# Optimization experiments

Measured on AMD Instinct MI355X. Metric: run time of the kernel, lower is better.

Reference implementation:

```python
import jax, jax.numpy as jnp
import numpy as np

B, S, D, H = 4, 2048, 512, 8
KD = D // H          # key_dim == head_dim == 64
FFN = 4 * D

def _ln(x, g, b, eps):
    mu = x.mean(-1, keepdims=True)
    var = ((x - mu) ** 2).mean(-1, keepdims=True)
    return (x - mu) / jnp.sqrt(var + eps) * g + b

def setup_inputs():
    key = jax.random.key(0)
    ks = jax.random.split(key, 8)
    def lin(k, o, i, scale=0.02):
        k1, k2 = jax.random.split(k)
        return (jax.random.normal(k1, (o, i), jnp.float32) * scale,
                jax.random.normal(k2, (o,), jnp.float32) * scale)
    wq, bq = lin(ks[0], D, D)
    wk, bk = lin(ks[1], D, D)
    wv, bv = lin(ks[2], D, D)
    wg, bg = lin(ks[3], D, D)
    wo, bo = lin(ks[4], D, D)
    fc1_w, fc1_b = lin(ks[5], FFN, D)
    fc2_w, fc2_b = lin(ks[6], D, FFN)
    return {
        'src': jax.random.normal(ks[7], (B, S, D), jnp.float32),
        'mask': jnp.zeros((S, S), jnp.bool_),
        'padding_mask': jnp.zeros((B, S), jnp.bool_),
        'wq': wq, 'bq': bq, 'wk': wk, 'bk': bk, 'wv': wv, 'bv': bv,
        'wg': wg, 'bg': bg, 'wo': wo, 'bo': bo,
        'fc1_w': fc1_w, 'fc1_b': fc1_b, 'fc2_w': fc2_w, 'fc2_b': fc2_b,
        'ln_ffn_g': jnp.ones((FFN,), jnp.float32), 'ln_ffn_b': jnp.zeros((FFN,), jnp.float32),
        'n0_g': jnp.ones((D,), jnp.float32), 'n0_b': jnp.zeros((D,), jnp.float32),
        'n1_g': jnp.ones((D,), jnp.float32), 'n1_b': jnp.zeros((D,), jnp.float32),
    }

def reference(src, mask, padding_mask, wq, bq, wk, bk, wv, bv, wg, bg, wo, bo,
              fc1_w, fc1_b, fc2_w, fc2_b, ln_ffn_g, ln_ffn_b, n0_g, n0_b, n1_g, n1_b):
    b, s, d = src.shape
    # RetNet per-head decay mask (h, s, s): exp((i-j)*log(gamma_h)) on the lower triangle,
    # row-normalized by sqrt(row sum) (torchscale RetNetRelPos, parallel mode).
    idx = jnp.arange(s)
    diff = (idx[:, None] - idx[None, :]).astype(src.dtype)
    decay = jnp.log(1.0 - 2.0 ** (-5.0 - jnp.arange(H, dtype=src.dtype)))
    dm = jnp.where(diff[None] >= 0, jnp.exp(diff[None] * decay[:, None, None]), 0.0)
    dm = dm / jnp.sqrt(dm.sum(-1, keepdims=True))
    # projections; k scaled by key_dim**-0.5 before head split
    q = (src @ wq.T + bq).reshape(b, s, H, KD).transpose(0, 2, 1, 3)
    k = ((src @ wk.T + bk) * (KD ** -0.5)).reshape(b, s, H, KD).transpose(0, 2, 1, 3)
    v = src @ wv.T + bv
    g = src @ wg.T + bg
    # parallel retention: additive decay bias, detached L1 row normalization
    qk = jnp.einsum('bhid,bhjd->bhij', q, k) + dm[None]
    den = jnp.maximum(jnp.abs(jax.lax.stop_gradient(qk).sum(-1, keepdims=True)), 1.0)
    qk = qk / den
    vr = v.reshape(b, s, H, KD).transpose(0, 2, 1, 3)
    o = jnp.einsum('bhij,bhjd->bhid', qk, vr).transpose(0, 2, 1, 3)  # (b,s,h,hd)
    # per-head LayerNorm, eps=1e-6, no affine
    mu = o.mean(-1, keepdims=True)
    o = (o - mu) / jnp.sqrt(((o - mu) ** 2).mean(-1, keepdims=True) + 1e-6)
    o = jax.nn.silu(g) * o.reshape(b, s, d)
    o = o @ wo.T + bo
    # post-norm residual layout
    x = _ln(src + o, n0_g, n0_b, 1e-5)
    h = jax.nn.gelu(x @ fc1_w.T + fc1_b, approximate=False)
    h = _ln(h, ln_ffn_g, ln_ffn_b, 1e-6)  # subln
    h = h @ fc2_w.T + fc2_b
    return _ln(x + h, n1_g, n1_b, 1e-5)
```

## Files before the change

kernel.cpp:

```cpp
#include <hip/hip_runtime.h>
#include <hip/hip_bf16.h>
#include <math.h>

#define DEV __device__ __forceinline__

typedef __attribute__((ext_vector_type(4))) float f32x4;
typedef __attribute__((ext_vector_type(16))) float f32x16;
typedef __attribute__((ext_vector_type(8))) short bf16x8;
typedef __attribute__((ext_vector_type(8))) unsigned short u16x8;
typedef unsigned short u16;
typedef unsigned int u32;

DEV u16 f2bf(float f) {
  union { float f; u32 u; } v; v.f = f;
  u32 r = v.u + 0x7fffu + ((v.u >> 16) & 1u);
  return (u16)(r >> 16);
}
DEV float bf2f(u16 h) {
  union { u32 u; float f; } v; v.u = ((u32)h) << 16;
  return v.f;
}
DEV float bfel(bf16x8 v, int e) {
  union { bf16x8 b; u16x8 u; } x; x.b = v; return bf2f(x.u[e]);
}

DEV void gl_lds16(const u16* g, u16* s) {
  __builtin_amdgcn_global_load_lds((const __attribute__((address_space(1))) void*)g,
                                   (__attribute__((address_space(3))) void*)s, 16, 0, 0);
}

DEV void barrier_() {
  __builtin_amdgcn_sched_barrier(0);
  asm volatile("" ::: "memory");
  __builtin_amdgcn_s_barrier();
  asm volatile("" ::: "memory");
  __builtin_amdgcn_sched_barrier(0);
}

#define MFMA16(a, b, c) __builtin_amdgcn_mfma_f32_16x16x32_bf16((a), (b), (c), 0, 0, 0)
#define MFMA32(a, b, c) __builtin_amdgcn_mfma_f32_32x32x16_bf16((a), (b), (c), 0, 0, 0)

DEV void cast8(const float* in, u16* out, float s) {
  f32x4 a = *(const f32x4*)in;
  f32x4 b = *(const f32x4*)(in + 4);
  u16x8 r;
  r[0] = f2bf(a[0] * s); r[1] = f2bf(a[1] * s); r[2] = f2bf(a[2] * s); r[3] = f2bf(a[3] * s);
  r[4] = f2bf(b[0] * s); r[5] = f2bf(b[1] * s); r[6] = f2bf(b[2] * s); r[7] = f2bf(b[3] * s);
  *(u16x8*)out = r;
}

__global__ __launch_bounds__(256) void prep_cast(
    const float* __restrict__ src, const float* __restrict__ wq, const float* __restrict__ wk,
    const float* __restrict__ wv, const float* __restrict__ wg, const float* __restrict__ wo,
    const float* __restrict__ fc1, const float* __restrict__ fc2,
    const float* __restrict__ bq, const float* __restrict__ bk,
    const float* __restrict__ bv, const float* __restrict__ bg,
    u16* __restrict__ src_bf, u16* __restrict__ Wcat, u16* __restrict__ wo_bf,
    u16* __restrict__ fc1_bf, u16* __restrict__ fc2_bf, float* __restrict__ bcat) {
  int u = blockIdx.x * 256 + threadIdx.x;
  if (u < 524288) {
    cast8(src + (size_t)u * 8, src_bf + (size_t)u * 8, 1.0f);
  } else if (u < 557056) {
    int v = u - 524288; cast8(wq + (size_t)v * 8, Wcat + (size_t)v * 8, 1.0f);
  } else if (u < 589824) {
    int v = u - 557056; cast8(wk + (size_t)v * 8, Wcat + 262144 + (size_t)v * 8, 0.125f);
  } else if (u < 622592) {
    int v = u - 589824; cast8(wv + (size_t)v * 8, Wcat + 524288 + (size_t)v * 8, 1.0f);
  } else if (u < 655360) {
    int v = u - 622592; cast8(wg + (size_t)v * 8, Wcat + 786432 + (size_t)v * 8, 1.0f);
  } else if (u < 688128) {
    int v = u - 655360; cast8(wo + (size_t)v * 8, wo_bf + (size_t)v * 8, 1.0f);
  } else if (u < 819200) {
    int v = u - 688128; cast8(fc1 + (size_t)v * 8, fc1_bf + (size_t)v * 8, 1.0f);
  } else if (u < 950272) {
    int v = u - 819200; cast8(fc2 + (size_t)v * 8, fc2_bf + (size_t)v * 8, 1.0f);
  } else if (u < 950528) {
    int v = u - 950272;
    #pragma unroll
    for (int e = 0; e < 8; e++) {
      int c = v * 8 + e;
      float val;
      if (c < 512)       val = bq[c];
      else if (c < 1024) val = bk[c - 512] * 0.125f;
      else if (c < 1536) val = bv[c - 1024];
      else               val = bg[c - 1536];
      bcat[c] = val;
    }
  }
}

template <int ACT>
__global__ __launch_bounds__(256) void gemm_v3(
    const u16* __restrict__ A, const u16* __restrict__ W, const float* __restrict__ bias,
    u16* __restrict__ Ob, int N, int K, int TN) {
  __shared__ __align__(16) u16 sm[2][16384];
  const int t = threadIdx.x, l = t & 63;
  const int w = t >> 6, wr = (w >> 1) * 64, wc = (w & 1) * 64;
  const int lc = l & 15, lch = l >> 4;
  const int NT = K >> 6;

  const int orig = blockIdx.x;
  const int cpx = gridDim.x >> 3;
  const int sid = (orig & 7) * cpx + (orig >> 3);
  const int bm = (sid / TN) * 128, bn = (sid % TN) * 128;

  const int srow = t >> 3, sc8 = t & 7;
  const u16* stA = A + (size_t)(bm + srow) * K + ((sc8 ^ (srow & 7)) * 8);
  const u16* stB = W + (size_t)(bn + srow) * K + ((sc8 ^ (srow & 7)) * 8);

#define STAGE(bidx, kt)                                                        \
  {                                                                            \
    u16* d = (u16*)sm[bidx] + t * 8;                                           \
    _Pragma("unroll")                                                          \
    for (int j = 0; j < 4; j++)                                                \
      gl_lds16(stA + (size_t)j * 32 * K + (kt), d + j * 2048);                 \
    _Pragma("unroll")                                                          \
    for (int j = 0; j < 4; j++)                                                \
      gl_lds16(stB + (size_t)j * 32 * K + (kt), d + 8192 + j * 2048);          \
  }

  f32x4 acc[4][4] = {};

  STAGE(0, 0)

  for (int tt = 0; tt < NT; ++tt) {
    if (tt + 1 < NT) {
      STAGE((tt + 1) & 1, (tt + 1) * 64)
      asm volatile("s_waitcnt vmcnt(8)" ::: "memory");
    } else {
      asm volatile("s_waitcnt vmcnt(0)" ::: "memory");
    }
    barrier_();
    const u16* bufp = sm[tt & 1];
    bf16x8 af[4][2], bfv[4][2];
    #pragma unroll
    for (int mi = 0; mi < 4; mi++) {
      const int row = wr + mi * 16 + lc;
      #pragma unroll
      for (int ks = 0; ks < 2; ks++) {
        const int ch = ks * 4 + lch;
        af[mi][ks] = *(const bf16x8*)&bufp[row * 64 + ((ch ^ (row & 7)) * 8)];
      }
    }
    #pragma unroll
    for (int ni = 0; ni < 4; ni++) {
      const int row = wc + ni * 16 + lc;
      #pragma unroll
      for (int ks = 0; ks < 2; ks++) {
        const int ch = ks * 4 + lch;
        bfv[ni][ks] = *(const bf16x8*)&bufp[8192 + row * 64 + ((ch ^ (row & 7)) * 8)];
      }
    }
    #pragma unroll
    for (int ks = 0; ks < 2; ks++)
      #pragma unroll
      for (int mi = 0; mi < 4; mi++)
        #pragma unroll
        for (int ni = 0; ni < 4; ni++)
          acc[mi][ni] = MFMA16(af[mi][ks], bfv[ni][ks], acc[mi][ni]);
    asm volatile("s_waitcnt lgkmcnt(0)" ::: "memory");
    barrier_();
  }
#undef STAGE

  u16* osm = (u16*)sm;
  #pragma unroll
  for (int ni = 0; ni < 4; ni++) {
    const int col = wc + ni * 16 + lc;
    const float bb = bias[bn + col];
    const int ckey = col >> 3, clow = col & 7;
    #pragma unroll
    for (int mi = 0; mi < 4; mi++) {
      #pragma unroll
      for (int r = 0; r < 4; r++) {
        const int row = wr + mi * 16 + lch * 4 + r;
        float v = acc[mi][ni][r] + bb;
        if (ACT == 1) v = 0.5f * v * (1.0f + erff(v * 0.70710678118f));
        osm[row * 128 + ((ckey ^ ((row & 7) << 1)) << 3) + clow] = f2bf(v);
      }
    }
  }
  __syncthreads();
  #pragma unroll
  for (int p = 0; p < 8; p++) {
    const int flat = p * 256 + t;
    const int row = flat >> 4, c = flat & 15;
    u16x8 y = *(const u16x8*)&osm[row * 128 + ((c ^ ((row & 7) << 1)) << 3)];
    *(u16x8*)&Ob[(size_t)(bm + row) * N + bn + c * 8] = y;
  }
}

template <int ACT>
__global__ __launch_bounds__(256) void gemm_m64(
    const u16* __restrict__ A, const u16* __restrict__ W, const float* __restrict__ bias,
    u16* __restrict__ Ob, int N, int K, int TN) {
  __shared__ __align__(16) u16 sm[2][12288];
  const int t = threadIdx.x, l = t & 63;
  const int w = t >> 6, wr = (w >> 1) * 32, wc = (w & 1) * 64;
  const int lc = l & 15, lch = l >> 4;
  const int NT = K >> 6;

  const int orig = blockIdx.x;
  const int cpx = gridDim.x >> 3;
  const int sid = (orig & 7) * cpx + (orig >> 3);
  const int bm = (sid / TN) * 64, bn = (sid % TN) * 128;

  const int srow = t >> 3, sc8 = t & 7;
  const u16* stA = A + (size_t)(bm + srow) * K + ((sc8 ^ (srow & 7)) * 8);
  const u16* stB = W + (size_t)(bn + srow) * K + ((sc8 ^ (srow & 7)) * 8);

#define STAGE(bidx, kt)                                                        \
  {                                                                            \
    u16* d = (u16*)sm[bidx] + t * 8;                                           \
    _Pragma("unroll")                                                          \
    for (int j = 0; j < 2; j++)                                                \
      gl_lds16(stA + (size_t)j * 32 * K + (kt), d + j * 2048);                 \
    _Pragma("unroll")                                                          \
    for (int j = 0; j < 4; j++)                                                \
      gl_lds16(stB + (size_t)j * 32 * K + (kt), d + 4096 + j * 2048);          \
  }

  f32x4 acc[2][4] = {};

  STAGE(0, 0)

  for (int tt = 0; tt < NT; ++tt) {
    if (tt + 1 < NT) {
      STAGE((tt + 1) & 1, (tt + 1) * 64)
      asm volatile("s_waitcnt vmcnt(6)" ::: "memory");
    } else {
      asm volatile("s_waitcnt vmcnt(0)" ::: "memory");
    }
    barrier_();
    const u16* bufp = sm[tt & 1];
    bf16x8 af[2][2], bfv[4][2];
    #pragma unroll
    for (int mi = 0; mi < 2; mi++) {
      const int row = wr + mi * 16 + lc;
      #pragma unroll
      for (int ks = 0; ks < 2; ks++) {
        const int ch = ks * 4 + lch;
        af[mi][ks] = *(const bf16x8*)&bufp[row * 64 + ((ch ^ (row & 7)) * 8)];
      }
    }
    #pragma unroll
    for (int ni = 0; ni < 4; ni++) {
      const int row = wc + ni * 16 + lc;
      #pragma unroll
      for (int ks = 0; ks < 2; ks++) {
        const int ch = ks * 4 + lch;
        bfv[ni][ks] = *(const bf16x8*)&bufp[4096 + row * 64 + ((ch ^ (row & 7)) * 8)];
      }
    }
    #pragma unroll
    for (int ks = 0; ks < 2; ks++)
      #pragma unroll
      for (int mi = 0; mi < 2; mi++)
        #pragma unroll
        for (int ni = 0; ni < 4; ni++)
          acc[mi][ni] = MFMA16(af[mi][ks], bfv[ni][ks], acc[mi][ni]);
    asm volatile("s_waitcnt lgkmcnt(0)" ::: "memory");
    barrier_();
  }
#undef STAGE

  u16* osm = (u16*)sm;
  #pragma unroll
  for (int ni = 0; ni < 4; ni++) {
    const int col = wc + ni * 16 + lc;
    const float bb = bias[bn + col];
    const int ckey = col >> 3, clow = col & 7;
    #pragma unroll
    for (int mi = 0; mi < 2; mi++) {
      #pragma unroll
      for (int r = 0; r < 4; r++) {
        const int row = wr + mi * 16 + lch * 4 + r;
        float v = acc[mi][ni][r] + bb;
        if (ACT == 1) v = 0.5f * v * (1.0f + erff(v * 0.70710678118f));
        osm[row * 128 + ((ckey ^ ((row & 7) << 1)) << 3) + clow] = f2bf(v);
      }
    }
  }
  __syncthreads();
  #pragma unroll
  for (int p = 0; p < 4; p++) {
    const int flat = p * 256 + t;
    const int row = flat >> 4, c = flat & 15;
    u16x8 y = *(const u16x8*)&osm[row * 128 + ((c ^ ((row & 7) << 1)) << 3)];
    *(u16x8*)&Ob[(size_t)(bm + row) * N + bn + c * 8] = y;
  }
}

__global__ __launch_bounds__(256) void transkv(
    const u16* __restrict__ qkvg, u16* __restrict__ ktg, u16* __restrict__ vtg,
    float* __restrict__ Wtab) {
  __shared__ u16 Lk[64 * 72], Lv[64 * 72];
  const int t = threadIdx.x;
  const int bh = blockIdx.x, c = blockIdx.y, b = bh >> 3, h = bh & 7;
  const int jt = c * 64;
  const u16* kptr = qkvg + (size_t)(b * 2048 + jt) * 2048 + 512 + h * 64;
  const u16* vptr = kptr + 512;
  const int r0 = t >> 3, c0 = (t & 7) * 8;
  u16x8 k0 = *(const u16x8*)(kptr + (size_t)r0 * 2048 + c0);
  u16x8 k1 = *(const u16x8*)(kptr + (size_t)(r0 + 32) * 2048 + c0);
  u16x8 v0 = *(const u16x8*)(vptr + (size_t)r0 * 2048 + c0);
  u16x8 v1 = *(const u16x8*)(vptr + (size_t)(r0 + 32) * 2048 + c0);
  #pragma unroll
  for (int e = 0; e < 8; e++) {
    Lk[(c0 + e) * 72 + r0] = k0[e];  Lk[(c0 + e) * 72 + 32 + r0] = k1[e];
    Lv[(c0 + e) * 72 + r0] = v0[e];  Lv[(c0 + e) * 72 + 32 + r0] = v1[e];
  }
  __syncthreads();
  {
    u16* kd = ktg + (size_t)bh * 64 * 2048 + jt;
    u16* vd = vtg + (size_t)bh * 64 * 2048 + jt;
    *(u16x8*)(kd + (size_t)r0 * 2048 + c0)        = *(const u16x8*)&Lk[r0 * 72 + c0];
    *(u16x8*)(kd + (size_t)(r0 + 32) * 2048 + c0) = *(const u16x8*)&Lk[(r0 + 32) * 72 + c0];
    *(u16x8*)(vd + (size_t)r0 * 2048 + c0)        = *(const u16x8*)&Lv[r0 * 72 + c0];
    *(u16x8*)(vd + (size_t)(r0 + 32) * 2048 + c0) = *(const u16x8*)&Lv[(r0 + 32) * 72 + c0];
  }
  if (t < 64) {
    const float gamma = 1.0f - exp2f(-5.0f - (float)h);
    float acc = 0.0f, p = 1.0f;
    for (int jj = 0; jj < 64; jj++) {
      acc += p * bf2f(Lv[t * 72 + (63 - jj)]);
      p *= gamma;
    }
    Wtab[((size_t)bh * 32 + c) * 64 + t] = acc;
  }
}

__global__ __launch_bounds__(256) void scanvtk(
    const u16* __restrict__ ktg, const u16* __restrict__ vtg,
    float* __restrict__ Ctab, float* __restrict__ ksum, u16* __restrict__ vtk) {
  __shared__ float red[3][4096];
  const int t = threadIdx.x, l = t & 63, w = t >> 6;
  const int bh = blockIdx.x, h = bh & 7;
  const int lc = l & 15, lch = l >> 4;

  {
    const int a = t & 63, q = t >> 6;
    const u16* kr = ktg + (size_t)bh * 64 * 2048 + (size_t)a * 2048 + q * 512;
    float s = 0.0f;
    for (int j = 0; j < 512; j += 8) {
      u16x8 v = *(const u16x8*)(kr + j);
      #pragma unroll
      for (int e = 0; e < 8; e++) s += bf2f(v[e]);
    }
    red[0][q * 64 + a] = s;
  }
  __syncthreads();
  if (t < 64) {
    ksum[bh * 64 + t] = red[0][t] + red[0][64 + t] + red[0][128 + t] + red[0][192 + t];
    const float gamma = 1.0f - exp2f(-5.0f - (float)h);
    const float g64 = exp2f(64.0f * log2f(gamma));
    float* Wp = Ctab + (size_t)bh * 32 * 64 + t;
    float C = 0.0f;
    for (int c = 0; c < 32; c++) {
      C = C * g64 + Wp[c * 64];
      Wp[c * 64] = C;
    }
  }

  const u16* vb = vtg + (size_t)bh * 64 * 2048;
  const u16* kb = ktg + (size_t)bh * 64 * 2048;
  f32x4 acc[4][4] = {};
  for (int it = 0; it < 16; ++it) {
    const int j0 = w * 512 + it * 32 + lch * 8;
    bf16x8 af[4], bfr[4];
    #pragma unroll
    for (int mt = 0; mt < 4; mt++)
      af[mt] = *(const bf16x8*)(vb + (size_t)(mt * 16 + lc) * 2048 + j0);
    #pragma unroll
    for (int nt = 0; nt < 4; nt++)
      bfr[nt] = *(const bf16x8*)(kb + (size_t)(nt * 16 + lc) * 2048 + j0);
    #pragma unroll
    for (int mt = 0; mt < 4; mt++)
      #pragma unroll
      for (int nt = 0; nt < 4; nt++)
        acc[mt][nt] = MFMA16(af[mt], bfr[nt], acc[mt][nt]);
  }
  __syncthreads();
  if (w > 0) {
    #pragma unroll
    for (int mt = 0; mt < 4; mt++)
      #pragma unroll
      for (int nt = 0; nt < 4; nt++)
        #pragma unroll
        for (int r = 0; r < 4; r++)
          red[w - 1][(mt * 16 + lch * 4 + r) * 64 + nt * 16 + lc] = acc[mt][nt][r];
  }
  __syncthreads();
  if (w == 0) {
    u16* out = vtk + (size_t)bh * 64 * 64;
    #pragma unroll
    for (int mt = 0; mt < 4; mt++)
      #pragma unroll
      for (int nt = 0; nt < 4; nt++)
        #pragma unroll
        for (int r = 0; r < 4; r++) {
          int row = mt * 16 + lch * 4 + r, col = nt * 16 + lc;
          float v = acc[mt][nt][r] + red[0][row * 64 + col] + red[1][row * 64 + col] +
                    red[2][row * 64 + col];
          out[row * 64 + col] = f2bf(v);
        }
  }
}

__global__ __launch_bounds__(512) void ret_out(
    const u16* __restrict__ qkvg, const u16* __restrict__ vtg,
    const u16* __restrict__ vtk, const float* __restrict__ Ctab,
    const float* __restrict__ ksum, u16* __restrict__ gated) {
  const int S = 2048, DD = 2048;
  const int bh = blockIdx.x, b = bh >> 3, h = bh & 7;
  const int t = threadIdx.x, l = t & 63, w = t >> 6;
  const int lid = l & 31, hi = l >> 5;
  const int wrow = blockIdx.y * 256 + w * 32;
  const int i_q = wrow + lid;
  const int chunk = wrow >> 6;
  const int iloc = i_q & 63;

  __shared__ __align__(16) u16 sm[18432];
  float* smf = (float*)sm;

  const size_t base = (size_t)b * S * DD + (size_t)h * 64;
  const u16* qp = qkvg + base;
  const u16* gp = qkvg + base + 1536;

  const float gamma = 1.0f - exp2f(-5.0f - (float)h);
  const float l2g = log2f(gamma);
  const float rowsum = (1.0f - exp2f((float)(i_q + 1) * l2g)) * exp2f(5.0f + (float)h);
  const float rrs = rsqrtf(rowsum);

  {
    const int il = t >> 3, j0 = (t & 7) * 8;
    u16x8 row;
    #pragma unroll
    for (int e = 0; e < 8; e++) {
      int d = il - (j0 + e);
      row[e] = (d >= 0) ? f2bf(exp2f((float)d * l2g)) : (u16)0;
    }
    *(u16x8*)&sm[il * 72 + j0] = row;
  }
  if (t < 256) {
    int cc = blockIdx.y * 4 - 1 + (t >> 6);
    smf[4608 + t] = (cc >= 0) ? Ctab[((size_t)bh * 32 + cc) * 64 + (t & 63)] : 0.0f;
  } else if (t < 320) {
    smf[4864 + (t - 256)] = ksum[bh * 64 + (t - 256)];
  }
  __syncthreads();

  bf16x8 qf[4];
  #pragma unroll
  for (int kc = 0; kc < 4; kc++)
    qf[kc] = *(const bf16x8*)(qp + (size_t)i_q * DD + kc * 16 + 8 * hi);

  const u16* vt_b = vtg + (size_t)bh * 64 * S;
  const u16* vk_b = vtk + (size_t)bh * 64 * 64;

  f32x16 accO0, accO1;
  #pragma unroll
  for (int r = 0; r < 16; r++) { accO0[r] = 0.0f; accO1[r] = 0.0f; }

  #pragma unroll
  for (int kc = 0; kc < 4; kc++) {
    bf16x8 lb = *(const bf16x8*)&sm[iloc * 72 + kc * 16 + hi * 8];
    bf16x8 va0 = *(const bf16x8*)(vt_b + (size_t)lid * S + chunk * 64 + kc * 16 + hi * 8);
    bf16x8 va1 = *(const bf16x8*)(vt_b + (size_t)(lid + 32) * S + chunk * 64 + kc * 16 + hi * 8);
    accO0 = MFMA32(va0, lb, accO0);
    accO1 = MFMA32(va1, lb, accO1);
  }
  {
    const float gpw = exp2f((float)(iloc + 1) * l2g);
    const float* Cst = &smf[4608 + (w >> 1) * 64];
    #pragma unroll
    for (int r = 0; r < 16; r++) {
      int br = (r & 3) + 8 * (r >> 2) + 4 * hi;
      accO0[r] += gpw * Cst[br];
      accO1[r] += gpw * Cst[32 + br];
    }
  }
  #pragma unroll
  for (int r = 0; r < 16; r++) { accO0[r] *= rrs; accO1[r] *= rrs; }
  #pragma unroll
  for (int kc = 0; kc < 4; kc++) {
    bf16x8 ka0 = *(const bf16x8*)(vk_b + (size_t)lid * 64 + kc * 16 + hi * 8);
    bf16x8 ka1 = *(const bf16x8*)(vk_b + (size_t)(lid + 32) * 64 + kc * 16 + hi * 8);
    accO0 = MFMA32(ka0, qf[kc], accO0);
    accO1 = MFMA32(ka1, qf[kc], accO1);
  }
  float dsum = 0.0f;
  #pragma unroll
  for (int kc = 0; kc < 4; kc++) {
    const float* Ks = &smf[4864 + kc * 16 + hi * 8];
    #pragma unroll
    for (int e = 0; e < 8; e++) dsum += bfel(qf[kc], e) * Ks[e];
  }
  dsum += __shfl_xor(dsum, 32);
  float den = dsum + sqrtf(rowsum);
  float rden = 1.0f / fmaxf(fabsf(den), 1.0f);

  float o0[16], o1[16];
  float s1 = 0.0f, s2 = 0.0f;
  #pragma unroll
  for (int r = 0; r < 16; r++) {
    o0[r] = accO0[r] * rden; s1 += o0[r]; s2 += o0[r] * o0[r];
    o1[r] = accO1[r] * rden; s1 += o1[r]; s2 += o1[r] * o1[r];
  }
  s1 += __shfl_xor(s1, 32);
  s2 += __shfl_xor(s2, 32);
  float mu = s1 * (1.0f / 64.0f);
  float var = s2 * (1.0f / 64.0f) - mu * mu;
  float rv = rsqrtf(var + 1e-6f);

  __syncthreads();

  u16* Ot = sm + w * 2304;
  #pragma unroll
  for (int r = 0; r < 16; r++) {
    int d = (r & 3) + 8 * (r >> 2) + 4 * hi;
    Ot[lid * 72 + d]      = f2bf((o0[r] - mu) * rv);
    Ot[lid * 72 + 32 + d] = f2bf((o1[r] - mu) * rv);
  }
  {
    const int i2 = l >> 1, half = l & 1;
    const int row = wrow + i2;
    #pragma unroll
    for (int c = 0; c < 4; c++) {
      u16x8 y8 = *(const u16x8*)&Ot[i2 * 72 + half * 32 + c * 8];
      u16x8 g8 = *(const u16x8*)(gp + (size_t)row * DD + half * 32 + c * 8);
      u16x8 o8;
      #pragma unroll
      for (int e = 0; e < 8; e++) {
        float gv = bf2f(g8[e]);
        float sg = gv / (1.0f + __expf(-gv));
        o8[e] = f2bf(bf2f(y8[e]) * sg);
      }
      *(u16x8*)&gated[((size_t)(b * S + row)) * 512 + h * 64 + half * 32 + c * 8] = o8;
    }
  }
}

template <int AF32, int WF>
__global__ __launch_bounds__(256) void add_lnT(
    const void* __restrict__ Ap, const u16* __restrict__ Bv,
    const float* __restrict__ gam, const float* __restrict__ bet, float eps,
    float* __restrict__ Of, u16* __restrict__ Ob) {
  int row = blockIdx.x * 4 + (threadIdx.x >> 6);
  int l = threadIdx.x & 63;
  float x[8];
  u16x8 cv = *(const u16x8*)(Bv + (size_t)row * 512 + l * 8);
  if (AF32) {
    const float* a = (const float*)Ap + (size_t)row * 512 + l * 8;
    f32x4 a0 = *(const f32x4*)a, a1 = *(const f32x4*)(a + 4);
    #pragma unroll
    for (int e = 0; e < 4; e++) { x[e] = a0[e] + bf2f(cv[e]); x[4 + e] = a1[e] + bf2f(cv[4 + e]); }
  } else {
    u16x8 av = *(const u16x8*)((const u16*)Ap + (size_t)row * 512 + l * 8);
    #pragma unroll
    for (int e = 0; e < 8; e++) x[e] = bf2f(av[e]) + bf2f(cv[e]);
  }
  float s = 0.f, s2 = 0.f;
  #pragma unroll
  for (int e = 0; e < 8; e++) { s += x[e]; s2 += x[e] * x[e]; }
  #pragma unroll
  for (int m = 1; m <= 32; m <<= 1) { s += __shfl_xor(s, m); s2 += __shfl_xor(s2, m); }
  float mu = s * (1.0f / 512.0f);
  float var = s2 * (1.0f / 512.0f) - mu * mu;
  float rinv = rsqrtf(var + eps);
  f32x4 g0 = *(const f32x4*)(gam + l * 8), g1 = *(const f32x4*)(gam + l * 8 + 4);
  f32x4 b0 = *(const f32x4*)(bet + l * 8), b1 = *(const f32x4*)(bet + l * 8 + 4);
  f32x4 y0, y1;
  #pragma unroll
  for (int e = 0; e < 4; e++) {
    y0[e] = (x[e] - mu) * rinv * g0[e] + b0[e];
    y1[e] = (x[4 + e] - mu) * rinv * g1[e] + b1[e];
  }
  if (WF) {
    float* op = Of + (size_t)row * 512 + l * 8;
    *(f32x4*)op = y0;
    *(f32x4*)(op + 4) = y1;
  }
  if (Ob) {
    u16x8 rb_;
    #pragma unroll
    for (int e = 0; e < 4; e++) { rb_[e] = f2bf(y0[e]); rb_[4 + e] = f2bf(y1[e]); }
    *(u16x8*)(Ob + (size_t)row * 512 + l * 8) = rb_;
  }
}

__global__ __launch_bounds__(256) void subln_ffn(
    u16* __restrict__ hbuf, const float* __restrict__ gam, const float* __restrict__ bet) {
  int row = blockIdx.x * 4 + (threadIdx.x >> 6);
  int l = threadIdx.x & 63;
  u16* p = hbuf + (size_t)row * 2048;
  float x[32];
  #pragma unroll
  for (int cch = 0; cch < 4; cch++) {
    u16x8 v = *(const u16x8*)(p + cch * 512 + l * 8);
    #pragma unroll
    for (int e = 0; e < 8; e++) x[cch * 8 + e] = bf2f(v[e]);
  }
  float s = 0.f, s2 = 0.f;
  #pragma unroll
  for (int e = 0; e < 32; e++) { s += x[e]; s2 += x[e] * x[e]; }
  #pragma unroll
  for (int m = 1; m <= 32; m <<= 1) { s += __shfl_xor(s, m); s2 += __shfl_xor(s2, m); }
  float mu = s * (1.0f / 2048.0f);
  float var = s2 * (1.0f / 2048.0f) - mu * mu;
  float rinv = rsqrtf(var + 1e-6f);
  #pragma unroll
  for (int cch = 0; cch < 4; cch++) {
    int col = cch * 512 + l * 8;
    f32x4 g0 = *(const f32x4*)(gam + col), g1 = *(const f32x4*)(gam + col + 4);
    f32x4 b0 = *(const f32x4*)(bet + col), b1 = *(const f32x4*)(bet + col + 4);
    u16x8 o;
    #pragma unroll
    for (int e = 0; e < 4; e++) {
      o[e]     = f2bf((x[cch * 8 + e]     - mu) * rinv * g0[e] + b0[e]);
      o[4 + e] = f2bf((x[cch * 8 + 4 + e] - mu) * rinv * g1[e] + b1[e]);
    }
    *(u16x8*)(p + col) = o;
  }
}

extern "C" void kernel_launch(void* const* d_in, const int* in_sizes, int n_in,
                              void* d_out, int out_size, void* d_ws, size_t ws_size,
                              hipStream_t stream) {
  const float* src  = (const float*)d_in[0];
  const float* wq   = (const float*)d_in[3];
  const float* bq   = (const float*)d_in[4];
  const float* wk   = (const float*)d_in[5];
  const float* bk   = (const float*)d_in[6];
  const float* wv   = (const float*)d_in[7];
  const float* bv   = (const float*)d_in[8];
  const float* wg   = (const float*)d_in[9];
  const float* bg   = (const float*)d_in[10];
  const float* wo   = (const float*)d_in[11];
  const float* bo   = (const float*)d_in[12];
  const float* fc1w = (const float*)d_in[13];
  const float* fc1b = (const float*)d_in[14];
  const float* fc2w = (const float*)d_in[15];
  const float* fc2b = (const float*)d_in[16];
  const float* lng  = (const float*)d_in[17];
  const float* lnb  = (const float*)d_in[18];
  const float* n0g  = (const float*)d_in[19];
  const float* n0b  = (const float*)d_in[20];
  const float* n1g  = (const float*)d_in[21];
  const float* n1b  = (const float*)d_in[22];

  if (ws_size < 91242496u) return;

  char* ws = (char*)d_ws;
  u16*   src_bf = (u16*)(ws + 0);
  u16*   Wcat   = (u16*)(ws + 8388608);
  u16*   wo_bf  = (u16*)(ws + 10485760);
  u16*   fc1_bf = (u16*)(ws + 11010048);
  u16*   fc2_bf = (u16*)(ws + 13107200);
  float* bcat   = (float*)(ws + 15204352);
  u16*   qkvg   = (u16*)(ws + 15212544);
  u16*   gated  = (u16*)(ws + 48766976);
  u16*   attn   = (u16*)(ws + 57155584);
  u16*   vtg    = (u16*)(ws + 65544192);
  u16*   ktg    = (u16*)(ws + 73932800);
  u16*   xbf    = (u16*)(ws + 82321408);
  float* Ctab   = (float*)(ws + 90710016);
  u16*   vtkb   = (u16*)(ws + 90972160);
  float* ksumb  = (float*)(ws + 91234304);

  prep_cast<<<3713, 256, 0, stream>>>(src, wq, wk, wv, wg, wo, fc1w, fc2w,
                                      bq, bk, bv, bg,
                                      src_bf, Wcat, wo_bf, fc1_bf, fc2_bf, bcat);
  gemm_v3<0><<<1024, 256, 0, stream>>>(src_bf, Wcat, bcat, qkvg, 2048, 512, 16);
  transkv<<<dim3(32, 32), 256, 0, stream>>>(qkvg, ktg, vtg, Ctab);
  scanvtk<<<32, 256, 0, stream>>>(ktg, vtg, Ctab, ksumb, vtkb);
  ret_out<<<dim3(32, 8), 512, 0, stream>>>(qkvg, vtg, vtkb, Ctab, ksumb, gated);
  gemm_m64<0><<<512, 256, 0, stream>>>(gated, wo_bf, bo, attn, 512, 512, 4);
  add_lnT<1, 0><<<2048, 256, 0, stream>>>(src, attn, n0g, n0b, 1e-5f, nullptr, xbf);
  gemm_v3<1><<<1024, 256, 0, stream>>>(xbf, fc1_bf, fc1b, qkvg, 2048, 512, 16);
  subln_ffn<<<2048, 256, 0, stream>>>(qkvg, lng, lnb);
  gemm_m64<0><<<512, 256, 0, stream>>>(qkvg, fc2_bf, fc2b, attn, 512, 2048, 4);
  add_lnT<0, 1><<<2048, 256, 0, stream>>>(xbf, attn, n1g, n1b, 1e-5f, (float*)d_out, nullptr);
}
```

Measured before the change: 178.9 us.

## Fuse K/V transpose into QKVG GEMM epilogue and move chunk decay sums into scan

The QKVG projection GEMM now writes its K and V column tiles directly in transposed (head, dim, seq) layout from shared memory, so the separate transkv kernel is removed. The per-chunk decayed V sums that transkv produced are now computed inside scanvtk from the transposed V. This saves a launch and one read/write pass over K and V. The cost is extra serial work in scanvtk, which runs only 32 blocks, and the K/V sections no longer get row-major output, which relies on nothing downstream reading K/V from qkvg.

```diff
diff --git a/kernel.cpp b/kernel.cpp
--- a/kernel.cpp
+++ b/kernel.cpp
@@ -89,10 +89,11 @@
   }
 }
 
-template <int ACT>
+template <int ACT, int TKV>
 __global__ __launch_bounds__(256) void gemm_v3(
     const u16* __restrict__ A, const u16* __restrict__ W, const float* __restrict__ bias,
-    u16* __restrict__ Ob, int N, int K, int TN) {
+    u16* __restrict__ Ob, u16* __restrict__ ktgp, u16* __restrict__ vtgp,
+    int N, int K, int TN) {
   __shared__ __align__(16) u16 sm[2][16384];
   const int t = threadIdx.x, l = t & 63;
   const int w = t >> 6, wr = (w >> 1) * 64, wc = (w & 1) * 64;
@@ -181,6 +182,30 @@
     }
   }
   __syncthreads();
+
+  if (TKV) {
+    const int sec = bn >> 9;
+    if (sec == 1 || sec == 2) {
+      u16* dst = (sec == 1) ? ktgp : vtgp;
+      const int bb2 = bm >> 11, s0 = bm & 2047;
+      const int hbase = (bn & 511) >> 6;
+      #pragma unroll
+      for (int pp = 0; pp < 8; pp++) {
+        const int pr = pp * 32 + (t >> 3);
+        const int col = pr >> 1, half = pr & 1, g = t & 7;
+        const int h = hbase + (col >> 6), d = col & 63;
+        const int ckey = col >> 3, clow = col & 7;
+        u16x8 v;
+        #pragma unroll
+        for (int e = 0; e < 8; e++) {
+          const int row = half * 64 + g * 8 + e;
+          v[e] = osm[row * 128 + ((ckey ^ (e << 1)) << 3) + clow];
+        }
+        *(u16x8*)(dst + ((size_t)((bb2 * 8 + h) * 64 + d)) * 2048 + s0 + half * 64 + g * 8) = v;
+      }
+      return;
+    }
+  }
   #pragma unroll
   for (int p = 0; p < 8; p++) {
     const int flat = p * 256 + t;
@@ -291,45 +316,6 @@
   }
 }
 
-__global__ __launch_bounds__(256) void transkv(
-    const u16* __restrict__ qkvg, u16* __restrict__ ktg, u16* __restrict__ vtg,
-    float* __restrict__ Wtab) {
-  __shared__ u16 Lk[64 * 72], Lv[64 * 72];
-  const int t = threadIdx.x;
-  const int bh = blockIdx.x, c = blockIdx.y, b = bh >> 3, h = bh & 7;
-  const int jt = c * 64;
-  const u16* kptr = qkvg + (size_t)(b * 2048 + jt) * 2048 + 512 + h * 64;
-  const u16* vptr = kptr + 512;
-  const int r0 = t >> 3, c0 = (t & 7) * 8;
-  u16x8 k0 = *(const u16x8*)(kptr + (size_t)r0 * 2048 + c0);
-  u16x8 k1 = *(const u16x8*)(kptr + (size_t)(r0 + 32) * 2048 + c0);
-  u16x8 v0 = *(const u16x8*)(vptr + (size_t)r0 * 2048 + c0);
-  u16x8 v1 = *(const u16x8*)(vptr + (size_t)(r0 + 32) * 2048 + c0);
-  #pragma unroll
-  for (int e = 0; e < 8; e++) {
-    Lk[(c0 + e) * 72 + r0] = k0[e];  Lk[(c0 + e) * 72 + 32 + r0] = k1[e];
-    Lv[(c0 + e) * 72 + r0] = v0[e];  Lv[(c0 + e) * 72 + 32 + r0] = v1[e];
-  }
-  __syncthreads();
-  {
-    u16* kd = ktg + (size_t)bh * 64 * 2048 + jt;
-    u16* vd = vtg + (size_t)bh * 64 * 2048 + jt;
-    *(u16x8*)(kd + (size_t)r0 * 2048 + c0)        = *(const u16x8*)&Lk[r0 * 72 + c0];
-    *(u16x8*)(kd + (size_t)(r0 + 32) * 2048 + c0) = *(const u16x8*)&Lk[(r0 + 32) * 72 + c0];
-    *(u16x8*)(vd + (size_t)r0 * 2048 + c0)        = *(const u16x8*)&Lv[r0 * 72 + c0];
-    *(u16x8*)(vd + (size_t)(r0 + 32) * 2048 + c0) = *(const u16x8*)&Lv[(r0 + 32) * 72 + c0];
-  }
-  if (t < 64) {
-    const float gamma = 1.0f - exp2f(-5.0f - (float)h);
-    float acc = 0.0f, p = 1.0f;
-    for (int jj = 0; jj < 64; jj++) {
-      acc += p * bf2f(Lv[t * 72 + (63 - jj)]);
-      p *= gamma;
-    }
-    Wtab[((size_t)bh * 32 + c) * 64 + t] = acc;
-  }
-}
-
 __global__ __launch_bounds__(256) void scanvtk(
     const u16* __restrict__ ktg, const u16* __restrict__ vtg,
     float* __restrict__ Ctab, float* __restrict__ ksum, u16* __restrict__ vtk) {
@@ -337,6 +323,7 @@
   const int t = threadIdx.x, l = t & 63, w = t >> 6;
   const int bh = blockIdx.x, h = bh & 7;
   const int lc = l & 15, lch = l >> 4;
+  const float gamma = 1.0f - exp2f(-5.0f - (float)h);
 
   {
     const int a = t & 63, q = t >> 6;
@@ -349,16 +336,32 @@
     }
     red[0][q * 64 + a] = s;
   }
+  {
+    const int d = t & 63, q = t >> 6;
+    const u16* vr = vtg + (size_t)bh * 64 * 2048 + (size_t)d * 2048;
+    for (int cc = 0; cc < 8; cc++) {
+      const int c = q * 8 + cc;
+      u16x8 vv[8];
+      #pragma unroll
+      for (int g = 0; g < 8; g++) vv[g] = *(const u16x8*)(vr + c * 64 + g * 8);
+      float acc = 0.0f, p = 1.0f;
+      #pragma unroll
+      for (int g = 7; g >= 0; g--) {
+        #pragma unroll
+        for (int e = 7; e >= 0; e--) { acc += p * bf2f(vv[g][e]); p *= gamma; }
+      }
+      red[0][512 + c * 64 + d] = acc;
+    }
+  }
   __syncthreads();
   if (t < 64) {
     ksum[bh * 64 + t] = red[0][t] + red[0][64 + t] + red[0][128 + t] + red[0][192 + t];
-    const float gamma = 1.0f - exp2f(-5.0f - (float)h);
     const float g64 = exp2f(64.0f * log2f(gamma));
-    float* Wp = Ctab + (size_t)bh * 32 * 64 + t;
     float C = 0.0f;
+    float* Cp = Ctab + (size_t)bh * 2048 + t;
     for (int c = 0; c < 32; c++) {
-      C = C * g64 + Wp[c * 64];
-      Wp[c * 64] = C;
+      C = C * g64 + red[0][512 + c * 64 + t];
+      Cp[c * 64] = C;
     }
   }
 
@@ -671,13 +674,14 @@
   prep_cast<<<3713, 256, 0, stream>>>(src, wq, wk, wv, wg, wo, fc1w, fc2w,
                                       bq, bk, bv, bg,
                                       src_bf, Wcat, wo_bf, fc1_bf, fc2_bf, bcat);
-  gemm_v3<0><<<1024, 256, 0, stream>>>(src_bf, Wcat, bcat, qkvg, 2048, 512, 16);
-  transkv<<<dim3(32, 32), 256, 0, stream>>>(qkvg, ktg, vtg, Ctab);
+  gemm_v3<0, 1><<<1024, 256, 0, stream>>>(src_bf, Wcat, bcat, qkvg, ktg, vtg,
+                                          2048, 512, 16);
   scanvtk<<<32, 256, 0, stream>>>(ktg, vtg, Ctab, ksumb, vtkb);
   ret_out<<<dim3(32, 8), 512, 0, stream>>>(qkvg, vtg, vtkb, Ctab, ksumb, gated);
   gemm_m64<0><<<512, 256, 0, stream>>>(gated, wo_bf, bo, attn, 512, 512, 4);
   add_lnT<1, 0><<<2048, 256, 0, stream>>>(src, attn, n0g, n0b, 1e-5f, nullptr, xbf);
-  gemm_v3<1><<<1024, 256, 0, stream>>>(xbf, fc1_bf, fc1b, qkvg, 2048, 512, 16);
+  gemm_v3<1, 0><<<1024, 256, 0, stream>>>(xbf, fc1_bf, fc1b, qkvg, nullptr, nullptr,
+                                          2048, 512, 16);
   subln_ffn<<<2048, 256, 0, stream>>>(qkvg, lng, lnb);
   gemm_m64<0><<<512, 256, 0, stream>>>(qkvg, fc2_bf, fc2b, attn, 512, 2048, 4);
   add_lnT<0, 1><<<2048, 256, 0, stream>>>(xbf, attn, n1g, n1b, 1e-5f, (float*)d_out, nullptr);
```

Result: slower. 186.4 us (+4.2%).
